# Performance work log

Hardware: AMD Instinct MI355X
Metric: run time of the kernel (lower is better)

Reference implementation:

```python
import jax, jax.numpy as jnp
import numpy as np

N = 65536   # nodes
E = 262144  # edges
IN = 16     # input node feat dim
H0 = 16     # layer0 out dim
H1 = 8      # layer1 out dim (H0 // 2)
EA = 10     # edge attr dim (hardcoded in edge_nn)


def setup_inputs() -> dict:
    key = jax.random.key(0)
    ks = jax.random.split(key, 12)
    s = 0.05
    return {
        "x": jax.random.normal(ks[0], (N, IN), jnp.float32),
        "edge_index": jax.random.randint(ks[1], (2, E), 0, N),
        "edge_attr": jax.random.normal(ks[2], (E, EA), jnp.float32),
        # layer 0 edge MLP: Linear(10, 256) -> ReLU -> Linear(256, IN*H0)
        "w1_0": jax.random.normal(ks[3], (EA, H0 * H0), jnp.float32) * s,
        "b1_0": jnp.zeros((H0 * H0,), jnp.float32),
        "w2_0": jax.random.normal(ks[4], (H0 * H0, IN * H0), jnp.float32) * s,
        "b2_0": jnp.zeros((IN * H0,), jnp.float32),
        "root_0": jax.random.normal(ks[5], (IN, H0), jnp.float32) * s,
        "bias_0": jnp.zeros((H0,), jnp.float32),
        # layer 1 edge MLP: Linear(10, 256) -> ReLU -> Linear(256, H0*H1)
        "w1_1": jax.random.normal(ks[6], (EA, H0 * H0), jnp.float32) * s,
        "b1_1": jnp.zeros((H0 * H0,), jnp.float32),
        "w2_1": jax.random.normal(ks[7], (H0 * H0, H0 * H1), jnp.float32) * s,
        "b2_1": jnp.zeros((H0 * H1,), jnp.float32),
        "root_1": jax.random.normal(ks[8], (H0, H1), jnp.float32) * s,
        "bias_1": jnp.zeros((H1,), jnp.float32),
        # final edge classifier fc: Linear(2*H1, 1)
        "fc_w": jax.random.normal(ks[9], (2 * H1, 1), jnp.float32) * s,
        "fc_b": jnp.zeros((1,), jnp.float32),
    }


def _nnconv(x, src, dst, edge_attr, w1, b1, w2, b2, root, bias, in_c, out_c):
    # edge-conditioned weight generation: MLP(edge_attr) -> [E, in_c, out_c]
    h = jax.nn.relu(edge_attr @ w1 + b1)                 # [E, hid]
    We = (h @ w2 + b2).reshape(-1, in_c, out_c)          # [E, in, out]
    msg = jnp.einsum('ei,eio->eo', x[src], We)           # per-edge matmul [E, out]
    ssum = jax.ops.segment_sum(msg, dst, num_segments=N)               # [N, out]
    cnt = jax.ops.segment_sum(jnp.ones((msg.shape[0],), msg.dtype), dst, num_segments=N)
    agg = ssum / jnp.maximum(cnt, 1.0)[:, None]          # scatter-mean
    return agg + x @ root + bias                         # root transform + bias


def reference(x, edge_index, edge_attr, w1_0, b1_0, w2_0, b2_0, root_0, bias_0,
              w1_1, b1_1, w2_1, b2_1, root_1, bias_1, fc_w, fc_b):
    src, dst = edge_index[0], edge_index[1]
    # dropout is identity in eval mode
    x = jax.nn.relu(_nnconv(x, src, dst, edge_attr, w1_0, b1_0, w2_0, b2_0, root_0, bias_0, IN, H0))
    x = jax.nn.relu(_nnconv(x, src, dst, edge_attr, w1_1, b1_1, w2_1, b2_1, root_1, bias_1, H0, H1))
    ef = jnp.concatenate([x[src], x[dst]], axis=-1)      # [E, 2*H1]
    return jax.nn.sigmoid(ef @ fc_w + fc_b)              # [E, 1]
```

## Files before the change

### kernel.cpp

```cpp
#include <hip/hip_runtime.h>
#include <stdint.h>

#define NN 65536
#define NE 262144

typedef __attribute__((ext_vector_type(8))) short bf16x8;
typedef __attribute__((ext_vector_type(4))) float f32x4;

__device__ __forceinline__ short f2bf(float f) {
  union { float f; uint32_t u; } v; v.f = f;
  uint32_t u = v.u + 0x7fffu + ((v.u >> 16) & 1u);
  return (short)(u >> 16);
}
__device__ __forceinline__ uint32_t cvtpk(float lo, float hi) {
  uint32_t r;
  asm("v_cvt_pk_bf16_f32 %0, %1, %2" : "=v"(r) : "v"(lo), "v"(hi));
  return r;
}

__global__ __launch_bounds__(256) void prep_all(
    const float* __restrict__ ea, short* __restrict__ eab,
    const float* __restrict__ w1_0, const float* __restrict__ w1_1,
    const float* __restrict__ w2_0, const float* __restrict__ w2_1,
    short* __restrict__ w1t0, short* __restrict__ w1t1,
    short* __restrict__ w2t0, short* __restrict__ w2t1,
    const int* __restrict__ ei, int* __restrict__ cnt32) {
  int idx = blockIdx.x * 256 + threadIdx.x;
  {
    int e = idx >> 4, k = idx & 15;
    eab[idx] = (k < 10) ? f2bf(ea[e * 10 + k]) : (short)0;
  }
  if (idx < NE) atomicAdd(&cnt32[ei[NE + idx]], 1);
  if (idx < 65536) {
    if (idx < 8192) {
      int n = idx >> 5, k = idx & 31;
      w1t0[idx] = (k < 10) ? f2bf(w1_0[k * 256 + n]) : (short)0;
      w1t1[idx] = (k < 10) ? f2bf(w1_1[k * 256 + n]) : (short)0;
    }
    if (idx < 32768) {
      int n = idx >> 8, k = idx & 255;
      w2t1[idx] = f2bf(w2_1[k * 128 + n]);
    }
    {
      int n = idx >> 8, k = idx & 255;
      w2t0[idx] = f2bf(w2_0[k * 256 + n]);
    }
  }
}

__global__ __launch_bounds__(256) void scan1_kernel(const int* __restrict__ cnt32,
                                                    int* __restrict__ bsum) {
  __shared__ int sd[256];
  int t = threadIdx.x, b = blockIdx.x;
  sd[t] = cnt32[b * 256 + t];
  __syncthreads();
  for (int s = 128; s > 0; s >>= 1) {
    if (t < s) sd[t] += sd[t + s];
    __syncthreads();
  }
  if (t == 0) bsum[b] = sd[0];
}

__global__ __launch_bounds__(256) void scan2_kernel(const int* __restrict__ bsum,
                                                    int* __restrict__ boff) {
  __shared__ int sd[256];
  int t = threadIdx.x;
  int v = bsum[t];
  sd[t] = v;
  __syncthreads();
  for (int st = 1; st < 256; st <<= 1) {
    int x = (t >= st) ? sd[t - st] : 0;
    __syncthreads();
    sd[t] += x;
    __syncthreads();
  }
  boff[t] = sd[t] - v;
}

__global__ __launch_bounds__(256) void scan3_kernel(const int* __restrict__ cnt32,
                                                    const int* __restrict__ boff,
                                                    int* __restrict__ off,
                                                    int* __restrict__ cursor) {
  __shared__ int sd[256];
  int t = threadIdx.x, b = blockIdx.x;
  int idx = b * 256 + t;
  int v = cnt32[idx];
  sd[t] = v;
  __syncthreads();
  for (int st = 1; st < 256; st <<= 1) {
    int x = (t >= st) ? sd[t - st] : 0;
    __syncthreads();
    sd[t] += x;
    __syncthreads();
  }
  int o = boff[b] + sd[t] - v;
  off[idx] = o;
  cursor[idx] = o;
  if (b == 255 && t == 255) off[65536] = boff[255] + sd[255];
}

__global__ __launch_bounds__(256) void scatter_kernel(const int* __restrict__ ei,
                                                      int* __restrict__ cursor,
                                                      int* __restrict__ eidx) {
  int e = blockIdx.x * 256 + threadIdx.x;
  int pos = atomicAdd(&cursor[ei[NE + e]], 1);
  eidx[pos] = e;
}

template <int N2, int OUTC>
__global__ __launch_bounds__(512, 4) void edge_kernel(
    const float* __restrict__ x, const int* __restrict__ ei,
    const short* __restrict__ eab, const short* __restrict__ w1t,
    const float* __restrict__ b1, const short* __restrict__ w2t,
    const float* __restrict__ b2, float* __restrict__ msg) {
  constexpr int WCOLS = N2 / 8;
  constexpr int NT2 = WCOLS / 16;
  constexpr int LOGO = (OUTC == 16) ? 4 : 3;
  constexpr int PADO = OUTC + 1;
  constexpr int PARTSZ = 8 * 128 * PADO * 4;
  constexpr int XSOFF = (PARTSZ > 65536) ? PARTSZ : 65536;
  __shared__ alignas(16) char smem[XSOFF + 128 * 20 * 4];
  short* const hB = (short*)smem;
  float* const partial = (float*)smem;
  float* const xs = (float*)(smem + XSOFF);

  const int tid = threadIdx.x;
  const int w = tid >> 6;
  const int lane = tid & 63;
  const int g = lane >> 4;
  const int lr = lane & 15;
  const int e0 = blockIdx.x * 128;

  const int eR = tid >> 2;
  const int qR = tid & 3;
  {
    int s = ei[e0 + eR];
    float4 v = *(const float4*)(x + (size_t)s * 16 + qR * 4);
    *(float4*)(xs + eR * 20 + qR * 4) = v;
  }

  bf16x8 aw[2];
#pragma unroll
  for (int ml = 0; ml < 2; ++ml)
    aw[ml] = *(const bf16x8*)(w1t + ((w * 2 + ml) * 16 + lr) * 32 + g * 8);
  bf16x8 be[8];
#pragma unroll
  for (int et = 0; et < 8; ++et) {
    if (g < 2)
      be[et] = *(const bf16x8*)(eab + (size_t)(e0 + et * 16 + lr) * 16 + g * 8);
    else
      be[et] = (bf16x8){0, 0, 0, 0, 0, 0, 0, 0};
  }

  f32x4 acc1[2][8];
#pragma unroll
  for (int ml = 0; ml < 2; ++ml)
#pragma unroll
    for (int et = 0; et < 8; ++et) acc1[ml][et] = (f32x4){0.f, 0.f, 0.f, 0.f};
#pragma unroll
  for (int et = 0; et < 8; ++et)
#pragma unroll
    for (int ml = 0; ml < 2; ++ml)
      acc1[ml][et] = __builtin_amdgcn_mfma_f32_16x16x32_bf16(aw[ml], be[et], acc1[ml][et], 0, 0, 0);

  bf16x8 bcur[NT2];
#pragma unroll
  for (int nt = 0; nt < NT2; ++nt) {
    int colo = w * WCOLS + nt * 16 + lr;
    bcur[nt] = *(const bf16x8*)(w2t + colo * 256 + g * 8);
  }

#pragma unroll
  for (int ml = 0; ml < 2; ++ml) {
    const int K16 = w * 2 + ml;
    const int rg = ml * 2 + (g >> 1);
    const int j0 = (g & 1) * 4;
    float4 bb1 = *(const float4*)(b1 + K16 * 16 + g * 4);
#pragma unroll
    for (int et = 0; et < 8; ++et) {
      float v0 = fmaxf(acc1[ml][et][0] + bb1.x, 0.f);
      float v1 = fmaxf(acc1[ml][et][1] + bb1.y, 0.f);
      float v2 = fmaxf(acc1[ml][et][2] + bb1.z, 0.f);
      float v3 = fmaxf(acc1[ml][et][3] + bb1.w, 0.f);
      int2 pw; pw.x = (int)cvtpk(v0, v1); pw.y = (int)cvtpk(v2, v3);
      *(int2*)(hB + ((et * 8 + w) * 64 + rg * 16 + lr) * 8 + j0) = pw;
    }
  }
  __syncthreads();

  f32x4 acc[8][NT2];
#pragma unroll
  for (int mt = 0; mt < 8; ++mt)
#pragma unroll
    for (int nt = 0; nt < NT2; ++nt) acc[mt][nt] = (f32x4){0.f, 0.f, 0.f, 0.f};
#pragma unroll
  for (int ks = 0; ks < 8; ++ks) {
    bf16x8 bnxt[NT2];
    if (ks < 7) {
#pragma unroll
      for (int nt = 0; nt < NT2; ++nt) {
        int colo = w * WCOLS + nt * 16 + lr;
        bnxt[nt] = *(const bf16x8*)(w2t + colo * 256 + (ks + 1) * 32 + g * 8);
      }
    }
#pragma unroll
    for (int hf = 0; hf < 2; ++hf) {
      bf16x8 a2[4];
#pragma unroll
      for (int m4 = 0; m4 < 4; ++m4)
        a2[m4] = *(const bf16x8*)(hB + (((hf * 4 + m4) * 8 + ks) * 64 + lane) * 8);
#pragma unroll
      for (int nt = 0; nt < NT2; ++nt)
#pragma unroll
        for (int m4 = 0; m4 < 4; ++m4)
          acc[hf * 4 + m4][nt] =
              __builtin_amdgcn_mfma_f32_16x16x32_bf16(a2[m4], bcur[nt], acc[hf * 4 + m4][nt], 0, 0, 0);
    }
    if (ks < 7) {
#pragma unroll
      for (int nt = 0; nt < NT2; ++nt) bcur[nt] = bnxt[nt];
    }
  }
  __syncthreads();

  {
    const int o = lr & (OUTC - 1);
    float b2c[NT2];
    int iv[NT2];
#pragma unroll
    for (int nt = 0; nt < NT2; ++nt) {
      int colo = w * WCOLS + nt * 16 + lr;
      b2c[nt] = b2[colo];
      iv[nt] = colo >> LOGO;
    }
#pragma unroll
    for (int mt = 0; mt < 8; ++mt)
#pragma unroll
      for (int r = 0; r < 4; ++r) {
        int e = mt * 16 + g * 4 + r;
        float m = 0.f;
#pragma unroll
        for (int nt = 0; nt < NT2; ++nt)
          m += (acc[mt][nt][r] + b2c[nt]) * xs[e * 20 + iv[nt]];
        if (OUTC == 8) m += __shfl_xor(m, 8, 64);
        partial[((size_t)w * 128 + e) * PADO + o] = m;
      }
  }
  __syncthreads();

  if (qR * 4 < OUTC) {
    float v[4];
#pragma unroll
    for (int j = 0; j < 4; ++j) {
      int o = qR * 4 + j;
      float s = 0.f;
#pragma unroll
      for (int sl = 0; sl < 8; ++sl) s += partial[((size_t)sl * 128 + eR) * PADO + o];
      v[j] = s;
    }
    *(float4*)(msg + (size_t)(e0 + eR) * OUTC + qR * 4) =
        (float4){v[0], v[1], v[2], v[3]};
  }
}

template <int OUTC>
__global__ __launch_bounds__(256) void node_csr(
    const float* __restrict__ xin, const float* __restrict__ msg,
    const int* __restrict__ off, const int* __restrict__ eidx,
    const float* __restrict__ root, const float* __restrict__ bias,
    float* __restrict__ xout) {
  constexpr int Q = OUTC / 4;
  __shared__ float rootL[16 * OUTC];
  __shared__ float biasL[OUTC];
  int tid = threadIdx.x;
  if (tid < 16 * OUTC) rootL[tid] = root[tid];
  if (tid < OUTC) biasL[tid] = bias[tid];
  __syncthreads();
  int n = blockIdx.x * (256 / Q) + tid / Q;
  int q = tid & (Q - 1);
  int o0 = off[n], o1 = off[n + 1];
  const float4* msg4 = (const float4*)msg;
  float s[4] = {0.f, 0.f, 0.f, 0.f};
  for (int i = o0; i < o1; ++i) {
    int e = eidx[i];
    float4 v = msg4[(size_t)e * Q + q];
    s[0] += v.x; s[1] += v.y; s[2] += v.z; s[3] += v.w;
  }
  float inv = 1.0f / fmaxf((float)(o1 - o0), 1.0f);
  float xi[16];
#pragma unroll
  for (int i = 0; i < 4; ++i) {
    float4 v = ((const float4*)(xin + (size_t)n * 16))[i];
    xi[4 * i] = v.x; xi[4 * i + 1] = v.y; xi[4 * i + 2] = v.z; xi[4 * i + 3] = v.w;
  }
  float r[4];
#pragma unroll
  for (int j = 0; j < 4; ++j) {
    int o = q * 4 + j;
    float a = s[j] * inv + biasL[o];
#pragma unroll
    for (int i = 0; i < 16; ++i) a += xi[i] * rootL[i * OUTC + o];
    r[j] = fmaxf(a, 0.f);
  }
  *(float4*)(xout + (size_t)n * OUTC + q * 4) = (float4){r[0], r[1], r[2], r[3]};
}

__global__ __launch_bounds__(256) void final_kernel(
    const float* __restrict__ x2, const int* __restrict__ ei,
    const float* __restrict__ fcw, const float* __restrict__ fcb,
    float* __restrict__ out) {
  int e = blockIdx.x * 256 + threadIdx.x;
  int s = ei[e], d = ei[NE + e];
  float acc = fcb[0];
  const float* xsr = x2 + (size_t)s * 8;
  const float* xdr = x2 + (size_t)d * 8;
#pragma unroll
  for (int c = 0; c < 8; ++c) acc += xsr[c] * fcw[c];
#pragma unroll
  for (int c = 0; c < 8; ++c) acc += xdr[c] * fcw[8 + c];
  out[e] = 1.0f / (1.0f + __expf(-acc));
}

extern "C" void kernel_launch(void* const* d_in, const int* in_sizes, int n_in,
                              void* d_out, int out_size, void* d_ws, size_t ws_size,
                              hipStream_t stream) {
  const float* x      = (const float*)d_in[0];
  const int*   ei     = (const int*)d_in[1];
  const float* ea     = (const float*)d_in[2];
  const float* w1_0   = (const float*)d_in[3];
  const float* b1_0   = (const float*)d_in[4];
  const float* w2_0   = (const float*)d_in[5];
  const float* b2_0   = (const float*)d_in[6];
  const float* root_0 = (const float*)d_in[7];
  const float* bias_0 = (const float*)d_in[8];
  const float* w1_1   = (const float*)d_in[9];
  const float* b1_1   = (const float*)d_in[10];
  const float* w2_1   = (const float*)d_in[11];
  const float* b2_1   = (const float*)d_in[12];
  const float* root_1 = (const float*)d_in[13];
  const float* bias_1 = (const float*)d_in[14];
  const float* fc_w   = (const float*)d_in[15];
  const float* fc_b   = (const float*)d_in[16];
  float* out = (float*)d_out;

  char* ws = (char*)d_ws;
  int*   off    = (int*)(ws);
  int*   cursor = (int*)(ws + (512u << 10));
  int*   bsum   = (int*)(ws + (1u << 20));
  int*   boff   = (int*)(ws + (1u << 20) + 4096);
  short* w1t0   = (short*)(ws + (1u << 20) + 16384);
  short* w1t1   = w1t0 + 8192;
  short* w2t0   = w1t1 + 8192;
  short* w2t1   = w2t0 + 65536;
  float* x1     = (float*)(ws + (2u << 20));
  float* x2     = (float*)(ws + (6u << 20));
  int*   eidx   = (int*)(ws + (8u << 20));
  short* eab    = (short*)(ws + (9u << 20));
  float* msg    = (float*)(ws + (17u << 20));

  int* cnt32 = cursor;

  hipMemsetAsync(cnt32, 0, (size_t)NN * 4, stream);
  prep_all<<<NE * 16 / 256, 256, 0, stream>>>(ea, eab, w1_0, w1_1, w2_0, w2_1,
                                              w1t0, w1t1, w2t0, w2t1, ei, cnt32);
  scan1_kernel<<<256, 256, 0, stream>>>(cnt32, bsum);
  scan2_kernel<<<1, 256, 0, stream>>>(bsum, boff);
  scan3_kernel<<<256, 256, 0, stream>>>(cnt32, boff, off, cursor);
  scatter_kernel<<<NE / 256, 256, 0, stream>>>(ei, cursor, eidx);

  edge_kernel<256, 16><<<NE / 128, 512, 0, stream>>>(
      x, ei, eab, w1t0, b1_0, w2t0, b2_0, msg);
  node_csr<16><<<NN * 4 / 256, 256, 0, stream>>>(x, msg, off, eidx, root_0, bias_0, x1);
  edge_kernel<128, 8><<<NE / 128, 512, 0, stream>>>(
      x1, ei, eab, w1t1, b1_1, w2t1, b2_1, msg);
  node_csr<8><<<NN * 2 / 256, 256, 0, stream>>>(x1, msg, off, eidx, root_1, bias_1, x2);
  final_kernel<<<NE / 256, 256, 0, stream>>>(x2, ei, fc_w, fc_b, out);
}
```

Baseline: 165.3 us.

## Halve edge tile to 64 edges and convert edge_attr to bf16 inline

Drops the separate pass that converted edge_attr into a padded bf16 buffer. Each edge kernel now reads the float attributes directly and packs them to bf16 itself. The edge tile also shrinks from 128 to 64 edges per block, which halves shared memory and the accumulator registers, and the occupancy hint is raised from 4 to 6 blocks. The aim is more resident waves and less prep traffic. The cost is twice as many blocks, each reloading the W2 weights with less reuse, and edge_attr being read unaligned twice.

Measured after the change: 213.5 us. 1.29x slower.

```diff
diff --git a/kernel.cpp b/kernel.cpp
--- a/kernel.cpp
+++ b/kernel.cpp
@@ -19,18 +19,13 @@
 }
 
 __global__ __launch_bounds__(256) void prep_all(
-    const float* __restrict__ ea, short* __restrict__ eab,
     const float* __restrict__ w1_0, const float* __restrict__ w1_1,
     const float* __restrict__ w2_0, const float* __restrict__ w2_1,
     short* __restrict__ w1t0, short* __restrict__ w1t1,
     short* __restrict__ w2t0, short* __restrict__ w2t1,
     const int* __restrict__ ei, int* __restrict__ cnt32) {
   int idx = blockIdx.x * 256 + threadIdx.x;
-  {
-    int e = idx >> 4, k = idx & 15;
-    eab[idx] = (k < 10) ? f2bf(ea[e * 10 + k]) : (short)0;
-  }
-  if (idx < NE) atomicAdd(&cnt32[ei[NE + idx]], 1);
+  atomicAdd(&cnt32[ei[NE + idx]], 1);
   if (idx < 65536) {
     if (idx < 8192) {
       int n = idx >> 5, k = idx & 31;
@@ -108,18 +103,18 @@
 }
 
 template <int N2, int OUTC>
-__global__ __launch_bounds__(512, 4) void edge_kernel(
+__global__ __launch_bounds__(512, 6) void edge_kernel(
     const float* __restrict__ x, const int* __restrict__ ei,
-    const short* __restrict__ eab, const short* __restrict__ w1t,
+    const float* __restrict__ ea, const short* __restrict__ w1t,
     const float* __restrict__ b1, const short* __restrict__ w2t,
     const float* __restrict__ b2, float* __restrict__ msg) {
   constexpr int WCOLS = N2 / 8;
   constexpr int NT2 = WCOLS / 16;
   constexpr int LOGO = (OUTC == 16) ? 4 : 3;
   constexpr int PADO = OUTC + 1;
-  constexpr int PARTSZ = 8 * 128 * PADO * 4;
-  constexpr int XSOFF = (PARTSZ > 65536) ? PARTSZ : 65536;
-  __shared__ alignas(16) char smem[XSOFF + 128 * 20 * 4];
+  constexpr int PARTSZ = 8 * 64 * PADO * 4;
+  constexpr int XSOFF = (PARTSZ > 32768) ? PARTSZ : 32768;
+  __shared__ alignas(16) char smem[XSOFF + 64 * 20 * 4];
   short* const hB = (short*)smem;
   float* const partial = (float*)smem;
   float* const xs = (float*)(smem + XSOFF);
@@ -129,36 +124,47 @@
   const int lane = tid & 63;
   const int g = lane >> 4;
   const int lr = lane & 15;
-  const int e0 = blockIdx.x * 128;
-
-  const int eR = tid >> 2;
-  const int qR = tid & 3;
-  {
-    int s = ei[e0 + eR];
-    float4 v = *(const float4*)(x + (size_t)s * 16 + qR * 4);
-    *(float4*)(xs + eR * 20 + qR * 4) = v;
+  const int e0 = blockIdx.x * 64;
+
+  if (tid < 256) {
+    int e = tid >> 2, q = tid & 3;
+    int s = ei[e0 + e];
+    float4 v = *(const float4*)(x + (size_t)s * 16 + q * 4);
+    *(float4*)(xs + e * 20 + q * 4) = v;
   }
 
   bf16x8 aw[2];
 #pragma unroll
   for (int ml = 0; ml < 2; ++ml)
     aw[ml] = *(const bf16x8*)(w1t + ((w * 2 + ml) * 16 + lr) * 32 + g * 8);
-  bf16x8 be[8];
-#pragma unroll
-  for (int et = 0; et < 8; ++et) {
-    if (g < 2)
-      be[et] = *(const bf16x8*)(eab + (size_t)(e0 + et * 16 + lr) * 16 + g * 8);
-    else
-      be[et] = (bf16x8){0, 0, 0, 0, 0, 0, 0, 0};
-  }
-
-  f32x4 acc1[2][8];
+  bf16x8 be[4];
+#pragma unroll
+  for (int et = 0; et < 4; ++et) {
+    union { bf16x8 v; uint32_t u[4]; } bu;
+    bu.v = (bf16x8){0, 0, 0, 0, 0, 0, 0, 0};
+    if (g < 2) {
+      const float* ep = ea + (size_t)(e0 + et * 16 + lr) * 10;
+      if (g == 0) {
+#pragma unroll
+        for (int j = 0; j < 4; ++j) {
+          float2 u = *(const float2*)(ep + j * 2);
+          bu.u[j] = cvtpk(u.x, u.y);
+        }
+      } else {
+        float2 u = *(const float2*)(ep + 8);
+        bu.u[0] = cvtpk(u.x, u.y);
+      }
+    }
+    be[et] = bu.v;
+  }
+
+  f32x4 acc1[2][4];
 #pragma unroll
   for (int ml = 0; ml < 2; ++ml)
 #pragma unroll
-    for (int et = 0; et < 8; ++et) acc1[ml][et] = (f32x4){0.f, 0.f, 0.f, 0.f};
-#pragma unroll
-  for (int et = 0; et < 8; ++et)
+    for (int et = 0; et < 4; ++et) acc1[ml][et] = (f32x4){0.f, 0.f, 0.f, 0.f};
+#pragma unroll
+  for (int et = 0; et < 4; ++et)
 #pragma unroll
     for (int ml = 0; ml < 2; ++ml)
       acc1[ml][et] = __builtin_amdgcn_mfma_f32_16x16x32_bf16(aw[ml], be[et], acc1[ml][et], 0, 0, 0);
@@ -177,7 +183,7 @@
     const int j0 = (g & 1) * 4;
     float4 bb1 = *(const float4*)(b1 + K16 * 16 + g * 4);
 #pragma unroll
-    for (int et = 0; et < 8; ++et) {
+    for (int et = 0; et < 4; ++et) {
       float v0 = fmaxf(acc1[ml][et][0] + bb1.x, 0.f);
       float v1 = fmaxf(acc1[ml][et][1] + bb1.y, 0.f);
       float v2 = fmaxf(acc1[ml][et][2] + bb1.z, 0.f);
@@ -188,9 +194,9 @@
   }
   __syncthreads();
 
-  f32x4 acc[8][NT2];
-#pragma unroll
-  for (int mt = 0; mt < 8; ++mt)
+  f32x4 acc[4][NT2];
+#pragma unroll
+  for (int mt = 0; mt < 4; ++mt)
 #pragma unroll
     for (int nt = 0; nt < NT2; ++nt) acc[mt][nt] = (f32x4){0.f, 0.f, 0.f, 0.f};
 #pragma unroll
@@ -203,19 +209,15 @@
         bnxt[nt] = *(const bf16x8*)(w2t + colo * 256 + (ks + 1) * 32 + g * 8);
       }
     }
-#pragma unroll
-    for (int hf = 0; hf < 2; ++hf) {
-      bf16x8 a2[4];
-#pragma unroll
-      for (int m4 = 0; m4 < 4; ++m4)
-        a2[m4] = *(const bf16x8*)(hB + (((hf * 4 + m4) * 8 + ks) * 64 + lane) * 8);
-#pragma unroll
-      for (int nt = 0; nt < NT2; ++nt)
-#pragma unroll
-        for (int m4 = 0; m4 < 4; ++m4)
-          acc[hf * 4 + m4][nt] =
-              __builtin_amdgcn_mfma_f32_16x16x32_bf16(a2[m4], bcur[nt], acc[hf * 4 + m4][nt], 0, 0, 0);
-    }
+    bf16x8 a2[4];
+#pragma unroll
+    for (int mt = 0; mt < 4; ++mt)
+      a2[mt] = *(const bf16x8*)(hB + ((mt * 8 + ks) * 64 + lane) * 8);
+#pragma unroll
+    for (int nt = 0; nt < NT2; ++nt)
+#pragma unroll
+      for (int mt = 0; mt < 4; ++mt)
+        acc[mt][nt] = __builtin_amdgcn_mfma_f32_16x16x32_bf16(a2[mt], bcur[nt], acc[mt][nt], 0, 0, 0);
     if (ks < 7) {
 #pragma unroll
       for (int nt = 0; nt < NT2; ++nt) bcur[nt] = bnxt[nt];
@@ -234,7 +236,7 @@
       iv[nt] = colo >> LOGO;
     }
 #pragma unroll
-    for (int mt = 0; mt < 8; ++mt)
+    for (int mt = 0; mt < 4; ++mt)
 #pragma unroll
       for (int r = 0; r < 4; ++r) {
         int e = mt * 16 + g * 4 + r;
@@ -243,23 +245,28 @@
         for (int nt = 0; nt < NT2; ++nt)
           m += (acc[mt][nt][r] + b2c[nt]) * xs[e * 20 + iv[nt]];
         if (OUTC == 8) m += __shfl_xor(m, 8, 64);
-        partial[((size_t)w * 128 + e) * PADO + o] = m;
+        partial[((size_t)w * 64 + e) * PADO + o] = m;
       }
   }
   __syncthreads();
 
-  if (qR * 4 < OUTC) {
-    float v[4];
-#pragma unroll
-    for (int j = 0; j < 4; ++j) {
-      int o = qR * 4 + j;
-      float s = 0.f;
-#pragma unroll
-      for (int sl = 0; sl < 8; ++sl) s += partial[((size_t)sl * 128 + eR) * PADO + o];
-      v[j] = s;
-    }
-    *(float4*)(msg + (size_t)(e0 + eR) * OUTC + qR * 4) =
-        (float4){v[0], v[1], v[2], v[3]};
+  {
+    int eR = tid >> 3;
+    int qR = tid & 7;
+    if (qR * 4 < OUTC) {
+      float v[4];
+#pragma unroll
+      for (int j = 0; j < 4; ++j) {
+        int o = qR * 4 + j;
+        float s = 0.f;
+#pragma unroll
+        for (int sl = 0; sl < 8; ++sl)
+          s += partial[((size_t)sl * 64 + eR) * PADO + o];
+        v[j] = s;
+      }
+      *(float4*)(msg + (size_t)(e0 + eR) * OUTC + qR * 4) =
+          (float4){v[0], v[1], v[2], v[3]};
+    }
   }
 }
 
@@ -355,24 +362,23 @@
   float* x1     = (float*)(ws + (2u << 20));
   float* x2     = (float*)(ws + (6u << 20));
   int*   eidx   = (int*)(ws + (8u << 20));
-  short* eab    = (short*)(ws + (9u << 20));
-  float* msg    = (float*)(ws + (17u << 20));
+  float* msg    = (float*)(ws + (9u << 20));
 
   int* cnt32 = cursor;
 
   hipMemsetAsync(cnt32, 0, (size_t)NN * 4, stream);
-  prep_all<<<NE * 16 / 256, 256, 0, stream>>>(ea, eab, w1_0, w1_1, w2_0, w2_1,
-                                              w1t0, w1t1, w2t0, w2t1, ei, cnt32);
+  prep_all<<<NE / 256, 256, 0, stream>>>(w1_0, w1_1, w2_0, w2_1,
+                                         w1t0, w1t1, w2t0, w2t1, ei, cnt32);
   scan1_kernel<<<256, 256, 0, stream>>>(cnt32, bsum);
   scan2_kernel<<<1, 256, 0, stream>>>(bsum, boff);
   scan3_kernel<<<256, 256, 0, stream>>>(cnt32, boff, off, cursor);
   scatter_kernel<<<NE / 256, 256, 0, stream>>>(ei, cursor, eidx);
 
-  edge_kernel<256, 16><<<NE / 128, 512, 0, stream>>>(
-      x, ei, eab, w1t0, b1_0, w2t0, b2_0, msg);
+  edge_kernel<256, 16><<<NE / 64, 512, 0, stream>>>(
+      x, ei, ea, w1t0, b1_0, w2t0, b2_0, msg);
   node_csr<16><<<NN * 4 / 256, 256, 0, stream>>>(x, msg, off, eidx, root_0, bias_0, x1);
-  edge_kernel<128, 8><<<NE / 128, 512, 0, stream>>>(
-      x1, ei, eab, w1t1, b1_1, w2t1, b2_1, msg);
+  edge_kernel<128, 8><<<NE / 64, 512, 0, stream>>>(
+      x1, ei, ea, w1t1, b1_1, w2t1, b2_1, msg);
   node_csr<8><<<NN * 2 / 256, 256, 0, stream>>>(x1, msg, off, eidx, root_1, bias_1, x2);
   final_kernel<<<NE / 256, 256, 0, stream>>>(x2, ei, fc_w, fc_b, out);
 }
```
